# Optimization experiments

Hardware: AMD Instinct MI355X
Metric: run time of the kernel (lower is better)

## Reference

```python
import jax, jax.numpy as jnp
import numpy as np

S, N, D = 8, 2048, 256

def setup_inputs() -> dict:
    key = jax.random.key(0)
    k0, k1, k2 = jax.random.split(key, 3)
    tensor0 = jax.random.normal(k0, (S, N, D), dtype=jnp.float32)
    tensor1 = jax.random.normal(k1, (S, N, D), dtype=jnp.float32)
    # glorot-ish scale for the (D, D) bilinear kernel
    kernel = jax.random.normal(k2, (D, D), dtype=jnp.float32) * (1.0 / np.sqrt(D))
    bias = jnp.zeros((1,), dtype=jnp.float32)  # scalar bias, shape () in keras
    return {"tensor0": tensor0, "tensor1": tensor1, "kernel": kernel, "bias": bias}

def reference(tensor0, tensor1, kernel, bias):
    # Faithful math of Bilinear(bilin_axes=[1]) on inputs [S, N, D]:
    # out[s, i, j] = sum_{d,e} tensor1[s,i,d] * kernel[d,e] * tensor0[s,j,e] + bias
    # (the original builds the full [S,N,S,N] cross tensor and extracts the
    #  batch diagonal; this einsum is the equivalent O(S*N*N*D) contraction).
    qt0 = jnp.einsum('de,sje->sjd', kernel, tensor0)      # [S, N, D]
    out = jnp.einsum('sid,sjd->sij', tensor1, qt0)        # [S, N, N]
    return out + bias[0]
```

## Files before the change

### kernel.cpp

```cpp
#include <hip/hip_runtime.h>
#include <hip/hip_bf16.h>


typedef __bf16 bf16x8 __attribute__((ext_vector_type(8)));
typedef float f32x4 __attribute__((ext_vector_type(4)));

__device__ __forceinline__ unsigned short f2bf(float f) {
  union { __hip_bfloat16 h; unsigned short u; } v;
  v.h = __float2bfloat16(f);
  return v.u;
}

__global__ __launch_bounds__(256) void cvt3(const float4* __restrict__ t0,
                                            const float4* __restrict__ t1,
                                            const float4* __restrict__ kk,
                                            ushort4* __restrict__ o0,
                                            ushort4* __restrict__ o1,
                                            ushort4* __restrict__ ok) {
  const int stride = gridDim.x * blockDim.x;
  const int i0 = blockIdx.x * blockDim.x + threadIdx.x;
  for (int j = i0; j < 1048576; j += stride) {
    float4 v = t0[j];
    o0[j] = make_ushort4(f2bf(v.x), f2bf(v.y), f2bf(v.z), f2bf(v.w));
  }
  for (int j = i0; j < 1048576; j += stride) {
    float4 v = t1[j];
    o1[j] = make_ushort4(f2bf(v.x), f2bf(v.y), f2bf(v.z), f2bf(v.w));
  }
  for (int j = i0; j < 16384; j += stride) {
    float4 v = kk[j];
    ok[j] = make_ushort4(f2bf(v.x), f2bf(v.y), f2bf(v.z), f2bf(v.w));
  }
}

template <bool OUT_BF16>
__global__ __launch_bounds__(256, 2) void gemm_nt(
    const unsigned short* __restrict__ A, const unsigned short* __restrict__ B,
    void* __restrict__ Cout, const float* __restrict__ bias,
    const int K, const int ldc,
    const long long aStride, const long long bStride, const long long cStride) {
  __shared__ unsigned short sA[128 * 32];
  __shared__ unsigned short sB[128 * 32];

  const int tid = threadIdx.x;
  const int wave = tid >> 6;
  const int lane = tid & 63;
  const int quad = lane >> 4;
  const int l16 = lane & 15;
  const int wrow = (wave >> 1) * 64;
  const int wcol = (wave & 1) * 64;

  const int brow = blockIdx.y * 128;
  const int bcol = blockIdx.x * 128;
  const long long bz = blockIdx.z;

  const unsigned short* Ab = A + bz * aStride + (long long)brow * K;
  const unsigned short* Bb = B + bz * bStride + (long long)bcol * K;

  const int srow = wave * 16 + (lane >> 2);
  const int scol = (lane & 3) * 8;

  f32x4 acc[4][4];
#pragma unroll
  for (int i = 0; i < 4; i++)
#pragma unroll
    for (int j = 0; j < 4; j++) acc[i][j] = (f32x4){0.f, 0.f, 0.f, 0.f};

  for (int kt = 0; kt < K; kt += 32) {
    __syncthreads();
#pragma unroll
    for (int half = 0; half < 2; half++) {
      const unsigned short* ga = Ab + (long long)(half * 64 + srow) * K + kt + scol;
      const unsigned short* gb = Bb + (long long)(half * 64 + srow) * K + kt + scol;
      unsigned short* la = &sA[(half * 64 + wave * 16) * 32];
      unsigned short* lb = &sB[(half * 64 + wave * 16) * 32];
      __builtin_amdgcn_global_load_lds(
          (const __attribute__((address_space(1))) unsigned int*)ga,
          (__attribute__((address_space(3))) unsigned int*)la, 16, 0, 0);
      __builtin_amdgcn_global_load_lds(
          (const __attribute__((address_space(1))) unsigned int*)gb,
          (__attribute__((address_space(3))) unsigned int*)lb, 16, 0, 0);
    }
    __syncthreads();

    bf16x8 af[4], bfr[4];
#pragma unroll
    for (int mi = 0; mi < 4; mi++)
      af[mi] = *(const bf16x8*)&sA[(wrow + mi * 16 + l16) * 32 + quad * 8];
#pragma unroll
    for (int ni = 0; ni < 4; ni++)
      bfr[ni] = *(const bf16x8*)&sB[(wcol + ni * 16 + l16) * 32 + quad * 8];
#pragma unroll
    for (int mi = 0; mi < 4; mi++)
#pragma unroll
      for (int ni = 0; ni < 4; ni++)
        acc[mi][ni] = __builtin_amdgcn_mfma_f32_16x16x32_bf16(af[mi], bfr[ni],
                                                              acc[mi][ni], 0, 0, 0);
  }

  if constexpr (OUT_BF16) {
    unsigned short* C = (unsigned short*)Cout + bz * cStride;
#pragma unroll
    for (int mi = 0; mi < 4; mi++)
#pragma unroll
      for (int ni = 0; ni < 4; ni++) {
        const int r0 = brow + wrow + mi * 16 + quad * 4;
        const int c = bcol + wcol + ni * 16 + l16;
#pragma unroll
        for (int r = 0; r < 4; r++)
          C[(long long)(r0 + r) * ldc + c] = f2bf(acc[mi][ni][r]);
      }
  } else {
    const float bv = bias[0];
    float* C = (float*)Cout + bz * cStride;
#pragma unroll
    for (int mi = 0; mi < 4; mi++)
#pragma unroll
      for (int ni = 0; ni < 4; ni++) {
        const int r0 = brow + wrow + mi * 16 + quad * 4;
        const int c = bcol + wcol + ni * 16 + l16;
#pragma unroll
        for (int r = 0; r < 4; r++)
          C[(long long)(r0 + r) * ldc + c] = acc[mi][ni][r] + bv;
      }
  }
}

extern "C" void kernel_launch(void* const* d_in, const int* in_sizes, int n_in,
                              void* d_out, int out_size, void* d_ws, size_t ws_size,
                              hipStream_t stream) {
  const float* t0 = (const float*)d_in[0];
  const float* t1 = (const float*)d_in[1];
  const float* kk = (const float*)d_in[2];
  const float* bias = (const float*)d_in[3];

  unsigned short* T0b = (unsigned short*)d_ws;
  unsigned short* T1b = T0b + 4194304;
  unsigned short* Kb = T1b + 4194304;
  unsigned short* Qb = Kb + 65536;

  cvt3<<<4096, 256, 0, stream>>>((const float4*)t0, (const float4*)t1,
                                 (const float4*)kk, (ushort4*)T0b,
                                 (ushort4*)T1b, (ushort4*)Kb);

  gemm_nt<true><<<dim3(2, 128, 1), 256, 0, stream>>>(T0b, Kb, Qb, nullptr, 256,
                                                     256, 0, 0, 0);

  gemm_nt<false><<<dim3(16, 16, 8), 256, 0, stream>>>(
      T1b, Qb, d_out, bias, 256, 2048, 524288LL, 524288LL, 4194304LL);
}
```

Measured before the change: 187.6 us.

## Double-buffer LDS tiles so global loads overlap MFMA in the GEMM

Splits the shared-memory A and B tiles into two buffers and unrolls the K loop by two. The next 32-wide K slice is issued with global_load_lds into the other buffer while the current one is read into registers and fed to MFMA. This aims to hide global-to-LDS load latency behind compute instead of waiting at a barrier on every step. It doubles LDS use per block, which may limit occupancy. The barrier still waits for outstanding loads, so overlap is limited to a single step.

```diff
diff --git a/kernel.cpp b/kernel.cpp
--- a/kernel.cpp
+++ b/kernel.cpp
@@ -39,8 +39,8 @@
     void* __restrict__ Cout, const float* __restrict__ bias,
     const int K, const int ldc,
     const long long aStride, const long long bStride, const long long cStride) {
-  __shared__ unsigned short sA[128 * 32];
-  __shared__ unsigned short sB[128 * 32];
+  __shared__ unsigned short sA[2][128 * 32];
+  __shared__ unsigned short sB[2][128 * 32];
 
   const int tid = threadIdx.x;
   const int wave = tid >> 6;
@@ -60,42 +60,65 @@
   const int srow = wave * 16 + (lane >> 2);
   const int scol = (lane & 3) * 8;
 
+  auto stage = [&](unsigned short* dA, unsigned short* dB, int kt) {
+#pragma unroll
+    for (int half = 0; half < 2; half++) {
+      const unsigned short* ga = Ab + (long long)(half * 64 + srow) * K + kt + scol;
+      const unsigned short* gb = Bb + (long long)(half * 64 + srow) * K + kt + scol;
+      __builtin_amdgcn_global_load_lds(
+          (const __attribute__((address_space(1))) unsigned int*)ga,
+          (__attribute__((address_space(3))) unsigned int*)(dA + (half * 64 + wave * 16) * 32),
+          16, 0, 0);
+      __builtin_amdgcn_global_load_lds(
+          (const __attribute__((address_space(1))) unsigned int*)gb,
+          (__attribute__((address_space(3))) unsigned int*)(dB + (half * 64 + wave * 16) * 32),
+          16, 0, 0);
+    }
+  };
+
   f32x4 acc[4][4];
 #pragma unroll
   for (int i = 0; i < 4; i++)
 #pragma unroll
     for (int j = 0; j < 4; j++) acc[i][j] = (f32x4){0.f, 0.f, 0.f, 0.f};
 
-  for (int kt = 0; kt < K; kt += 32) {
+  stage(sA[0], sB[0], 0);
+
+  for (int kt = 0; kt < K; kt += 64) {
     __syncthreads();
+    {
+      bf16x8 af[4], bfr[4];
 #pragma unroll
-    for (int half = 0; half < 2; half++) {
-      const unsigned short* ga = Ab + (long long)(half * 64 + srow) * K + kt + scol;
-      const unsigned short* gb = Bb + (long long)(half * 64 + srow) * K + kt + scol;
-      unsigned short* la = &sA[(half * 64 + wave * 16) * 32];
-      unsigned short* lb = &sB[(half * 64 + wave * 16) * 32];
-      __builtin_amdgcn_global_load_lds(
-          (const __attribute__((address_space(1))) unsigned int*)ga,
-          (__attribute__((address_space(3))) unsigned int*)la, 16, 0, 0);
-      __builtin_amdgcn_global_load_lds(
-          (const __attribute__((address_space(1))) unsigned int*)gb,
-          (__attribute__((address_space(3))) unsigned int*)lb, 16, 0, 0);
+      for (int mi = 0; mi < 4; mi++)
+        af[mi] = *(const bf16x8*)&sA[0][(wrow + mi * 16 + l16) * 32 + quad * 8];
+#pragma unroll
+      for (int ni = 0; ni < 4; ni++)
+        bfr[ni] = *(const bf16x8*)&sB[0][(wcol + ni * 16 + l16) * 32 + quad * 8];
+      stage(sA[1], sB[1], kt + 32);
+#pragma unroll
+      for (int mi = 0; mi < 4; mi++)
+#pragma unroll
+        for (int ni = 0; ni < 4; ni++)
+          acc[mi][ni] = __builtin_amdgcn_mfma_f32_16x16x32_bf16(
+              af[mi], bfr[ni], acc[mi][ni], 0, 0, 0);
     }
     __syncthreads();
-
-    bf16x8 af[4], bfr[4];
+    {
+      bf16x8 af[4], bfr[4];
 #pragma unroll
-    for (int mi = 0; mi < 4; mi++)
-      af[mi] = *(const bf16x8*)&sA[(wrow + mi * 16 + l16) * 32 + quad * 8];
-#pragma unroll
-    for (int ni = 0; ni < 4; ni++)
-      bfr[ni] = *(const bf16x8*)&sB[(wcol + ni * 16 + l16) * 32 + quad * 8];
-#pragma unroll
-    for (int mi = 0; mi < 4; mi++)
+      for (int mi = 0; mi < 4; mi++)
+        af[mi] = *(const bf16x8*)&sA[1][(wrow + mi * 16 + l16) * 32 + quad * 8];
 #pragma unroll
       for (int ni = 0; ni < 4; ni++)
-        acc[mi][ni] = __builtin_amdgcn_mfma_f32_16x16x32_bf16(af[mi], bfr[ni],
-                                                              acc[mi][ni], 0, 0, 0);
+        bfr[ni] = *(const bf16x8*)&sB[1][(wcol + ni * 16 + l16) * 32 + quad * 8];
+      if (kt + 64 < K) stage(sA[0], sB[0], kt + 64);
+#pragma unroll
+      for (int mi = 0; mi < 4; mi++)
+#pragma unroll
+        for (int ni = 0; ni < 4; ni++)
+          acc[mi][ni] = __builtin_amdgcn_mfma_f32_16x16x32_bf16(
+              af[mi], bfr[ni], acc[mi][ni], 0, 0, 0);
+    }
   }
 
   if constexpr (OUT_BF16) {
```

Measured after the change: 186.4 us. No clear change (-0.6%).
